# Kernel tuning notes

Hardware: AMD Instinct MI355X
Metric: run time of the kernel (lower is better)

## Reference

```python
import jax, jax.numpy as jnp
import numpy as np

PC_RANGE = [-51.2, -51.2, -5.0, 51.2, 51.2, 3.0]
NUM_HEADS, NUM_LEVELS, NUM_REFS, NUM_POINTS = 8, 4, 4, 1
EPS = 1e-5


def setup_inputs():
    key = jax.random.key(0)
    ks = jax.random.split(key, 16)
    B, CAMS, NQ, C, R = 1, 6, 10000, 256, NUM_REFS
    H, L, P = NUM_HEADS, NUM_LEVELS, NUM_POINTS
    shapes = np.array([[64, 160], [32, 80], [16, 40], [8, 20]], dtype=np.int64)
    hw = shapes[:, 0] * shapes[:, 1]
    lsi = np.concatenate([[0], np.cumsum(hw)[:-1]]).astype(np.int64)
    NK = int(hw.sum())

    def p(k, shape):
        return 0.02 * jax.random.normal(k, shape, jnp.float32)

    return {
        'query': jax.random.normal(ks[0], (NQ, B, C), jnp.float32),
        'query_pos': jax.random.normal(ks[1], (NQ, B, C), jnp.float32),
        'value': jax.random.normal(ks[2], (NK, B * CAMS, C), jnp.float32),
        'bev_reference_points': jax.random.uniform(ks[3], (B, NQ, R, 3), jnp.float32),
        'lidar2img': jax.random.normal(ks[4], (B, CAMS, 3, 4), jnp.float32),
        'img_shape': jnp.broadcast_to(jnp.array([512.0, 960.0], jnp.float32), (B, CAMS, 2)),
        'spatial_shapes': jnp.asarray(shapes),
        'level_start_index': jnp.asarray(lsi),
        'W_val': p(ks[5], (C, C)), 'b_val': jnp.zeros((C,), jnp.float32),
        'W_samp': p(ks[6], (C, H * L * R * P * 2)), 'b_samp': p(ks[7], (H * L * R * P * 2,)),
        'W_attn': p(ks[8], (C, H * L * R * P)), 'b_attn': jnp.zeros((H * L * R * P,), jnp.float32),
        'W_dout': p(ks[9], (C, C)), 'b_dout': jnp.zeros((C,), jnp.float32),
        'W_out': p(ks[10], (C, C)), 'b_out': jnp.zeros((C,), jnp.float32),
    }


def reference(query, query_pos, value, bev_reference_points, lidar2img, img_shape,
              spatial_shapes, level_start_index,
              W_val, b_val, W_samp, b_samp, W_attn, b_attn, W_dout, b_dout, W_out, b_out):
    shapes = np.asarray(spatial_shapes)
    lsi = np.asarray(level_start_index)
    H, L, R, P = NUM_HEADS, NUM_LEVELS, NUM_REFS, NUM_POINTS
    identity = query                                   # (NQ,B,C)
    q = jnp.transpose(query + query_pos, (1, 0, 2))    # (B,NQ,C)
    v = jnp.transpose(value, (1, 0, 2))                # (Bc,NK,C)
    B, NQ, C = q.shape
    CAMS = lidar2img.shape[1]
    Bc, dh = B * CAMS, C // H
    pc = jnp.asarray(PC_RANGE, q.dtype)

    # ---- project 3D reference points to each camera ----
    l2i = jnp.zeros((B, CAMS, 4, 4), q.dtype).at[..., 3, 3].set(1.0).at[..., :3, :4].set(lidar2img)
    xyz = bev_reference_points * (pc[3:6] - pc[0:3]) + pc[0:3]          # (B,NQ,R,3)
    pts = jnp.concatenate([xyz, jnp.ones_like(xyz[..., :1])], -1).reshape(B, NQ * R, 4)
    cam = jnp.einsum('bcij,bnj->bcni', l2i, pts)                         # (B,CAMS,NQ*R,4)
    z = cam[..., 2]
    xy = cam[..., :2] / jnp.maximum(z, EPS)[..., None]
    xy = xy / img_shape[:, :, None, ::-1]                                # x/w, y/h
    mask = (z > EPS) & (xy[..., 0] > 0.) & (xy[..., 0] < 1.) & (xy[..., 1] > 0.) & (xy[..., 1] < 1.)
    mask = mask.reshape(B, CAMS, NQ, R)
    ref_cam = xy.reshape(B, CAMS, NQ, R, 2)

    # rebatch: run attention for all queries per camera, mask outputs (same math as
    # gather-only-valid since deformable attention is pointwise per query)
    q_rb = jnp.broadcast_to(q[:, None], (B, CAMS, NQ, C)).reshape(Bc, NQ, C)
    rp_rb = ref_cam.reshape(Bc, NQ, R, 2)

    # ---- multi-scale deformable attention ----
    vproj = jnp.transpose((v @ W_val + b_val).reshape(Bc, -1, H, dh), (0, 2, 1, 3))  # (Bc,H,NK,dh)
    off = (q_rb @ W_samp + b_samp).reshape(Bc, NQ, H, L, R, P, 2)
    aw = jax.nn.softmax((q_rb @ W_attn + b_attn).reshape(Bc, NQ, H, L * R * P), -1)
    aw = aw.reshape(Bc, NQ, H, L, R, P)
    norm = jnp.asarray(shapes[:, ::-1].copy(), q.dtype)                  # (L,2) = (w,h)
    loc = rp_rb[:, :, None, None, :, None, :] + off / norm[None, None, None, :, None, None, :]

    acc = jnp.zeros((Bc, H, NQ, dh), q.dtype)
    for l in range(L):
        Hl, Wl, s = int(shapes[l, 0]), int(shapes[l, 1]), int(lsi[l])
        vf = vproj[:, :, s:s + Hl * Wl]                                  # (Bc,H,Hl*Wl,dh)

        def rs(t):  # (Bc,NQ,H,R,P) -> (Bc,H,M)
            return jnp.transpose(t, (0, 2, 1, 3, 4)).reshape(Bc, H, NQ * R * P)
        x = rs(loc[:, :, :, l, :, :, 0]) * Wl - 0.5   # grid_sample align_corners=False
        y = rs(loc[:, :, :, l, :, :, 1]) * Hl - 0.5
        w = rs(aw[:, :, :, l])
        x0 = jnp.floor(x); y0 = jnp.floor(y)
        lx = x - x0; ly = y - y0
        ix = x0.astype(jnp.int32); iy = y0.astype(jnp.int32)

        def g(iy_, ix_):  # zero-padding gather
            inb = (iy_ >= 0) & (iy_ < Hl) & (ix_ >= 0) & (ix_ < Wl)
            idx = jnp.clip(iy_, 0, Hl - 1) * Wl + jnp.clip(ix_, 0, Wl - 1)
            return jnp.take_along_axis(vf, idx[..., None], axis=2) * inb[..., None].astype(q.dtype)
        samp = (g(iy, ix) * ((1 - ly) * (1 - lx) * w)[..., None]
                + g(iy, ix + 1) * ((1 - ly) * lx * w)[..., None]
                + g(iy + 1, ix) * (ly * (1 - lx) * w)[..., None]
                + g(iy + 1, ix + 1) * (ly * lx * w)[..., None])            # (Bc,H,M,dh)
        acc = acc + samp.reshape(Bc, H, NQ, R * P, dh).sum(3)
    attn_out = jnp.transpose(acc, (0, 2, 1, 3)).reshape(Bc, NQ, C) @ W_dout + b_dout

    # ---- scatter/average valid camera contributions back to BEV slots ----
    valid = jnp.any(mask, -1)                                            # (B,CAMS,NQ)
    slots = jnp.sum(attn_out.reshape(B, CAMS, NQ, C) * valid[..., None].astype(q.dtype), 1)
    count = jnp.maximum(valid.sum(1).astype(q.dtype), 1.0)               # (B,NQ)
    slots = (slots / count[..., None]) @ W_out + b_out
    return jnp.transpose(slots, (1, 0, 2)) + identity
```

## Files before the change

### kernel.cpp

```cpp
#include <hip/hip_runtime.h>
#include <hip/hip_bf16.h>

namespace {

typedef unsigned short u16;
typedef unsigned int u32;
typedef unsigned char u8;
typedef __attribute__((ext_vector_type(8))) short bf16x8;
typedef __attribute__((ext_vector_type(4))) float f32x4;
typedef __attribute__((ext_vector_type(2))) float f32x2;

constexpr int kNQ   = 10000;
constexpr int kCams = 6;
constexpr int kC    = 256;
constexpr int kNK   = 13600;
constexpr float kEps = 1e-5f;

__device__ __forceinline__ u16 f2b(float f) {
  union { __hip_bfloat16 h; u16 u; } cv;
  cv.h = __float2bfloat16(f);
  return cv.u;
}
__device__ __forceinline__ float b2f(u16 b) {
  return __uint_as_float(((u32)b) << 16);
}
__device__ __forceinline__ bf16x8 pack8(const float4& a, const float4& b) {
  bf16x8 v;
  v[0] = (short)f2b(a.x); v[1] = (short)f2b(a.y);
  v[2] = (short)f2b(a.z); v[3] = (short)f2b(a.w);
  v[4] = (short)f2b(b.x); v[5] = (short)f2b(b.y);
  v[6] = (short)f2b(b.z); v[7] = (short)f2b(b.w);
  return v;
}
__device__ __forceinline__ u8 f2fp8(float v) {
  const u32 t = __builtin_amdgcn_cvt_pk_fp8_f32(v, 0.f, 0u, false);
  return (u8)(t & 0xffu);
}

__global__ __launch_bounds__(256) void k_cvt_w_all(
    const float* __restrict__ w_val, const float* __restrict__ w_samp,
    const float* __restrict__ w_attn, const float* __restrict__ w_dout,
    const float* __restrict__ w_out, u16* __restrict__ t_val,
    u16* __restrict__ t_sa, u16* __restrict__ t_dout, u16* __restrict__ t_out) {
  __shared__ float t[32][33];
  const int bn = blockIdx.x;
  const int bk = blockIdx.y;
  const int tid = threadIdx.x;
  const float* W; u16* Wt; int N, lb;
  if (bn < 8)       { W = w_val;  Wt = t_val;            N = 256; lb = bn; }
  else if (bn < 16) { W = w_samp; Wt = t_sa;             N = 256; lb = bn - 8; }
  else if (bn < 20) { W = w_attn; Wt = t_sa + 256 * 256; N = 128; lb = bn - 16; }
  else if (bn < 28) { W = w_dout; Wt = t_dout;           N = 256; lb = bn - 20; }
  else              { W = w_out;  Wt = t_out;            N = 256; lb = bn - 28; }
#pragma unroll
  for (int e = 0; e < 4; ++e) {
    const int i = e * 256 + tid;
    const int kk = i >> 5, nn = i & 31;
    t[kk][nn] = W[(bk * 32 + kk) * N + lb * 32 + nn];
  }
  __syncthreads();
#pragma unroll
  for (int e = 0; e < 4; ++e) {
    const int i = e * 256 + tid;
    const int nn = i >> 5, kk = i & 31;
    Wt[(lb * 32 + nn) * 256 + bk * 32 + kk] = f2b(t[kk][nn]);
  }
}

__global__ __launch_bounds__(256) void k_cvt_add(const float* __restrict__ a,
                                                 const float* __restrict__ b,
                                                 u16* __restrict__ out) {
  const int t = blockIdx.x * 256 + threadIdx.x;
  const int i = t * 8;
  const float4 x0 = *reinterpret_cast<const float4*>(a + i);
  const float4 x1 = *reinterpret_cast<const float4*>(a + i + 4);
  const float4 y0 = *reinterpret_cast<const float4*>(b + i);
  const float4 y1 = *reinterpret_cast<const float4*>(b + i + 4);
  float4 s0, s1;
  s0.x = x0.x + y0.x; s0.y = x0.y + y0.y; s0.z = x0.z + y0.z; s0.w = x0.w + y0.w;
  s1.x = x1.x + y1.x; s1.y = x1.y + y1.y; s1.z = x1.z + y1.z; s1.w = x1.w + y1.w;
  *reinterpret_cast<bf16x8*>(out + i) = pack8(s0, s1);
}

template <bool OUT_BF16, bool HAS_ADD>
__global__ __launch_bounds__(256) void k_mfma(const u16* __restrict__ A,
                                              const u16* __restrict__ Wt,
                                              const float* __restrict__ bias,
                                              const float* __restrict__ bias2,
                                              int nsplit,
                                              const float* __restrict__ bias_scale,
                                              const float* __restrict__ addend,
                                              void* __restrict__ outp,
                                              int M, int Ntot) {
  __shared__ u16 As[128 * 64];
  __shared__ u16 Bs[128 * 64];
  const int tid = threadIdx.x;
  const int m0 = blockIdx.x * 128;
  const int n0 = blockIdx.y * 128;
  const int wave = tid >> 6;
  const int lane = tid & 63;
  const int wr = wave >> 1;
  const int wc = wave & 1;
  const int lr = lane & 15;
  const int lg = lane >> 4;
  const int srow = tid >> 3;
  const int slot = tid & 7;

  const u16* aptr[4];
  const u16* bptr[4];
  int soff[4];
#pragma unroll
  for (int c = 0; c < 4; ++c) {
    const int rowA = c * 32 + srow;
    const int ra = min(m0 + rowA, M - 1);
    aptr[c] = A + (long long)ra * 256 + slot * 8;
    bptr[c] = Wt + (long long)(n0 + rowA) * 256 + slot * 8;
    soff[c] = rowA * 64 + ((slot ^ (rowA & 7)) << 3);
  }

  f32x4 acc[4][4] = {};

  bf16x8 ca[4], cb[4];
#pragma unroll
  for (int c = 0; c < 4; ++c) {
    ca[c] = *reinterpret_cast<const bf16x8*>(aptr[c]);
    cb[c] = *reinterpret_cast<const bf16x8*>(bptr[c]);
  }

#pragma unroll
  for (int kt = 0; kt < 4; ++kt) {
    bf16x8 na[4], nb[4];
    if (kt < 3) {
      const int k1 = (kt + 1) * 64;
#pragma unroll
      for (int c = 0; c < 4; ++c) {
        na[c] = *reinterpret_cast<const bf16x8*>(aptr[c] + k1);
        nb[c] = *reinterpret_cast<const bf16x8*>(bptr[c] + k1);
      }
    }
#pragma unroll
    for (int c = 0; c < 4; ++c) {
      *reinterpret_cast<bf16x8*>(&As[soff[c]]) = ca[c];
      *reinterpret_cast<bf16x8*>(&Bs[soff[c]]) = cb[c];
    }
    __syncthreads();
#pragma unroll
    for (int ks = 0; ks < 2; ++ks) {
      bf16x8 af[4], bfr[4];
#pragma unroll
      for (int mi = 0; mi < 4; ++mi) {
        const int r = wr * 64 + mi * 16 + lr;
        const int s = ks * 4 + lg;
        af[mi] = *reinterpret_cast<const bf16x8*>(&As[r * 64 + ((s ^ (r & 7)) << 3)]);
      }
#pragma unroll
      for (int ni = 0; ni < 4; ++ni) {
        const int r = wc * 64 + ni * 16 + lr;
        const int s = ks * 4 + lg;
        bfr[ni] = *reinterpret_cast<const bf16x8*>(&Bs[r * 64 + ((s ^ (r & 7)) << 3)]);
      }
#pragma unroll
      for (int mi = 0; mi < 4; ++mi)
#pragma unroll
        for (int ni = 0; ni < 4; ++ni)
          acc[mi][ni] = __builtin_amdgcn_mfma_f32_16x16x32_bf16(af[mi], bfr[ni],
                                                                acc[mi][ni], 0, 0, 0);
    }
    if (kt < 3) {
      __syncthreads();
#pragma unroll
      for (int c = 0; c < 4; ++c) { ca[c] = na[c]; cb[c] = nb[c]; }
    }
  }

#pragma unroll
  for (int mi = 0; mi < 4; ++mi) {
#pragma unroll
    for (int reg = 0; reg < 4; ++reg) {
      const int row = m0 + wr * 64 + mi * 16 + lg * 4 + reg;
      if (row < M) {
        const float bs = bias_scale ? bias_scale[row] : 1.f;
#pragma unroll
        for (int ni = 0; ni < 4; ++ni) {
          const int col = n0 + wc * 64 + ni * 16 + lr;
          const float b = (bias2 && col >= nsplit) ? bias2[col - nsplit] : bias[col];
          float v = acc[mi][ni][reg] + b * bs;
          if (HAS_ADD) v += addend[(long long)row * Ntot + col];
          if (OUT_BF16)
            ((u16*)outp)[(long long)row * Ntot + col] = f2b(v);
          else
            ((float*)outp)[(long long)row * Ntot + col] = v;
        }
      }
    }
  }
}

__global__ __launch_bounds__(256) void k_mfma_vproj(const float* __restrict__ value,
                                                    const u16* __restrict__ Wt,
                                                    const float* __restrict__ bias,
                                                    u8* __restrict__ outp) {
  constexpr int M = kNK * kCams;
  __shared__ u16 As[128 * 64];
  __shared__ u16 Bs[128 * 64];
  const int tid = threadIdx.x;
  const int m0 = blockIdx.x * 128;
  const int n0 = blockIdx.y * 128;
  const int wave = tid >> 6;
  const int lane = tid & 63;
  const int wr = wave >> 1;
  const int wc = wave & 1;
  const int lr = lane & 15;
  const int lg = lane >> 4;
  const int srow = tid >> 3;
  const int slot = tid & 7;

  const float* aptr[4];
  const u16* bptr[4];
  int soff[4];
#pragma unroll
  for (int c = 0; c < 4; ++c) {
    const int rowA = c * 32 + srow;
    const int g = min(m0 + rowA, M - 1);
    const int cam = g / kNK;
    const int n = g - cam * kNK;
    aptr[c] = value + (long long)(n * kCams + cam) * 256 + slot * 8;
    bptr[c] = Wt + (long long)(n0 + rowA) * 256 + slot * 8;
    soff[c] = rowA * 64 + ((slot ^ (rowA & 7)) << 3);
  }

  f32x4 acc[4][4] = {};

  float4 caf[8];
  bf16x8 cb[4];
#pragma unroll
  for (int c = 0; c < 4; ++c) {
    caf[2 * c]     = *reinterpret_cast<const float4*>(aptr[c]);
    caf[2 * c + 1] = *reinterpret_cast<const float4*>(aptr[c] + 4);
    cb[c] = *reinterpret_cast<const bf16x8*>(bptr[c]);
  }

#pragma unroll
  for (int kt = 0; kt < 4; ++kt) {
    float4 naf[8];
    bf16x8 nb[4];
    if (kt < 3) {
      const int k1 = (kt + 1) * 64;
#pragma unroll
      for (int c = 0; c < 4; ++c) {
        naf[2 * c]     = *reinterpret_cast<const float4*>(aptr[c] + k1);
        naf[2 * c + 1] = *reinterpret_cast<const float4*>(aptr[c] + k1 + 4);
        nb[c] = *reinterpret_cast<const bf16x8*>(bptr[c] + k1);
      }
    }
#pragma unroll
    for (int c = 0; c < 4; ++c) {
      *reinterpret_cast<bf16x8*>(&As[soff[c]]) = pack8(caf[2 * c], caf[2 * c + 1]);
      *reinterpret_cast<bf16x8*>(&Bs[soff[c]]) = cb[c];
    }
    __syncthreads();
#pragma unroll
    for (int ks = 0; ks < 2; ++ks) {
      bf16x8 af[4], bfr[4];
#pragma unroll
      for (int mi = 0; mi < 4; ++mi) {
        const int r = wr * 64 + mi * 16 + lr;
        const int s = ks * 4 + lg;
        af[mi] = *reinterpret_cast<const bf16x8*>(&As[r * 64 + ((s ^ (r & 7)) << 3)]);
      }
#pragma unroll
      for (int ni = 0; ni < 4; ++ni) {
        const int r = wc * 64 + ni * 16 + lr;
        const int s = ks * 4 + lg;
        bfr[ni] = *reinterpret_cast<const bf16x8*>(&Bs[r * 64 + ((s ^ (r & 7)) << 3)]);
      }
#pragma unroll
      for (int mi = 0; mi < 4; ++mi)
#pragma unroll
        for (int ni = 0; ni < 4; ++ni)
          acc[mi][ni] = __builtin_amdgcn_mfma_f32_16x16x32_bf16(af[mi], bfr[ni],
                                                                acc[mi][ni], 0, 0, 0);
    }
    if (kt < 3) {
      __syncthreads();
#pragma unroll
      for (int c = 0; c < 4; ++c) {
        caf[2 * c] = naf[2 * c];
        caf[2 * c + 1] = naf[2 * c + 1];
        cb[c] = nb[c];
      }
    }
  }

#pragma unroll
  for (int mi = 0; mi < 4; ++mi) {
#pragma unroll
    for (int reg = 0; reg < 4; ++reg) {
      const int row = m0 + wr * 64 + mi * 16 + lg * 4 + reg;
      if (row < M) {
#pragma unroll
        for (int ni = 0; ni < 4; ++ni) {
          const int col = n0 + wc * 64 + ni * 16 + lr;
          outp[(long long)row * 256 + col] = f2fp8(acc[mi][ni][reg] + bias[col]);
        }
      }
    }
  }
}

__global__ __launch_bounds__(128) void k_softmax16(float* __restrict__ offaw) {
  const int nq = blockIdx.x;
  const int t = threadIdx.x;
  float* p = offaw + (long long)nq * 384 + 256 + t;
  float v = *p;
  float mx = v;
#pragma unroll
  for (int s = 1; s < 16; s <<= 1) mx = fmaxf(mx, __shfl_xor(mx, s));
  const float e = expf(v - mx);
  float sm = e;
#pragma unroll
  for (int s = 1; s < 16; s <<= 1) sm += __shfl_xor(sm, s);
  *p = e / sm;
}

__global__ __launch_bounds__(256) void k_proj_ref(const float* __restrict__ refpts,
                                                  const float* __restrict__ l2i,
                                                  const float* __restrict__ img_shape,
                                                  float* __restrict__ refcam,
                                                  float* __restrict__ valid) {
  const int idx = blockIdx.x * blockDim.x + threadIdx.x;
  if (idx >= kCams * kNQ) return;
  const int cam = idx / kNQ;
  const int nq = idx - cam * kNQ;
  const float* Mp = l2i + cam * 12;
  float m[12];
#pragma unroll
  for (int i = 0; i < 12; ++i) m[i] = Mp[i];
  const float ih = img_shape[cam * 2 + 0];
  const float iw = img_shape[cam * 2 + 1];
  float anyv = 0.f;
  float* rcout = refcam + (long long)idx * 8;
#pragma unroll
  for (int r = 0; r < 4; ++r) {
    const float* rp = refpts + ((long long)nq * 4 + r) * 3;
    const float X = rp[0] * 102.4f + (-51.2f);
    const float Y = rp[1] * 102.4f + (-51.2f);
    const float Z = rp[2] * 8.0f + (-5.0f);
    const float cx = m[0] * X + m[1] * Y + m[2] * Z + m[3];
    const float cy = m[4] * X + m[5] * Y + m[6] * Z + m[7];
    const float cz = m[8] * X + m[9] * Y + m[10] * Z + m[11];
    const float zc = fmaxf(cz, kEps);
    const float xn = cx / zc / iw;
    const float yn = cy / zc / ih;
    rcout[r * 2 + 0] = xn;
    rcout[r * 2 + 1] = yn;
    if ((cz > kEps) && (xn > 0.f) && (xn < 1.f) && (yn > 0.f) && (yn < 1.f)) anyv = 1.f;
  }
  valid[idx] = anyv;
}

__global__ __launch_bounds__(64) void k_sample(const u8* __restrict__ vproj,
                                               const float* __restrict__ refcam,
                                               const float* __restrict__ offaw,
                                               const float* __restrict__ valid,
                                               u16* __restrict__ pre,
                                               float* __restrict__ cflag) {
  const int nq = blockIdx.x;
  const int lane = threadIdx.x;
  const int h = lane >> 3;
  const int d4 = lane & 7;

  static constexpr int SHH[4] = {64, 32, 16, 8};
  static constexpr int SHW[4] = {160, 80, 40, 20};
  static constexpr int LSI[4] = {0, 10240, 12800, 13440};

  const float* offp = offaw + (long long)nq * 384 + h * 32;
  const float* awp = offaw + (long long)nq * 384 + 256 + h * 16;

  float vl[kCams];
#pragma unroll
  for (int c = 0; c < kCams; ++c) vl[c] = valid[c * kNQ + nq];

  float4 acc4 = {0.f, 0.f, 0.f, 0.f};
  float count = 0.f;

  for (int cam = 0; cam < kCams; ++cam) {
    if (vl[cam] == 0.f) continue;
    count += 1.f;

    const float* rcp = refcam + (long long)(cam * kNQ + nq) * 8;
    const float4 rcA = *reinterpret_cast<const float4*>(rcp);
    const float4 rcB = *reinterpret_cast<const float4*>(rcp + 4);
    const float rx[4] = {rcA.x, rcA.z, rcB.x, rcB.z};
    const float ry[4] = {rcA.y, rcA.w, rcB.y, rcB.w};

#pragma unroll
    for (int l = 0; l < 4; ++l) {
      const int Hl = SHH[l];
      const int Wl = SHW[l];
      const float Hf = (float)Hl;
      const float Wf = (float)Wl;
      const float4 aw4 = *reinterpret_cast<const float4*>(awp + l * 4);
      const float4 ofA = *reinterpret_cast<const float4*>(offp + l * 8);
      const float4 ofB = *reinterpret_cast<const float4*>(offp + l * 8 + 4);
      const u8* vf = vproj + ((long long)(cam * kNK + LSI[l])) * 256 + h * 32 + d4 * 4;

      const float ox[4] = {ofA.x, ofA.z, ofB.x, ofB.z};
      const float oy[4] = {ofA.y, ofA.w, ofB.y, ofB.w};
      const float wr[4] = {aw4.x, aw4.y, aw4.z, aw4.w};

#pragma unroll
      for (int r = 0; r < 4; ++r) {
        const float x = fmaf(rx[r], Wf, ox[r]) - 0.5f;
        const float y = fmaf(ry[r], Hf, oy[r]) - 0.5f;
        const float x0 = floorf(x);
        const float y0 = floorf(y);
        const float lx = x - x0;
        const float ly = y - y0;
        const int ix = (int)x0;
        const int iy = (int)y0;
        const int ix0 = min(max(ix, 0), Wl - 1);
        const int ix1 = min(max(ix + 1, 0), Wl - 1);
        const int iy0 = min(max(iy, 0), Hl - 1);
        const int iy1 = min(max(iy + 1, 0), Hl - 1);
        const bool bx0 = (ix >= 0) & (ix < Wl);
        const bool bx1 = (ix >= -1) & (ix + 1 < Wl);
        const bool by0 = (iy >= 0) & (iy < Hl);
        const bool by1 = (iy >= -1) & (iy + 1 < Hl);
        const float w = wr[r];
        const float wy0 = w * (1.f - ly);
        const float wy1 = w * ly;
        const float w00 = (by0 && bx0) ? wy0 * (1.f - lx) : 0.f;
        const float w01 = (by0 && bx1) ? wy0 * lx : 0.f;
        const float w10 = (by1 && bx0) ? wy1 * (1.f - lx) : 0.f;
        const float w11 = (by1 && bx1) ? wy1 * lx : 0.f;
        const int q00 = *reinterpret_cast<const u32*>(vf + (iy0 * Wl + ix0) * 256);
        const int q01 = *reinterpret_cast<const u32*>(vf + (iy0 * Wl + ix1) * 256);
        const int q10 = *reinterpret_cast<const u32*>(vf + (iy1 * Wl + ix0) * 256);
        const int q11 = *reinterpret_cast<const u32*>(vf + (iy1 * Wl + ix1) * 256);
        const f32x2 a00 = __builtin_amdgcn_cvt_pk_f32_fp8(q00, false);
        const f32x2 b00 = __builtin_amdgcn_cvt_pk_f32_fp8(q00, true);
        const f32x2 a01 = __builtin_amdgcn_cvt_pk_f32_fp8(q01, false);
        const f32x2 b01 = __builtin_amdgcn_cvt_pk_f32_fp8(q01, true);
        const f32x2 a10 = __builtin_amdgcn_cvt_pk_f32_fp8(q10, false);
        const f32x2 b10 = __builtin_amdgcn_cvt_pk_f32_fp8(q10, true);
        const f32x2 a11 = __builtin_amdgcn_cvt_pk_f32_fp8(q11, false);
        const f32x2 b11 = __builtin_amdgcn_cvt_pk_f32_fp8(q11, true);
        acc4.x = fmaf(w00, a00[0], fmaf(w01, a01[0], fmaf(w10, a10[0], fmaf(w11, a11[0], acc4.x))));
        acc4.y = fmaf(w00, a00[1], fmaf(w01, a01[1], fmaf(w10, a10[1], fmaf(w11, a11[1], acc4.y))));
        acc4.z = fmaf(w00, b00[0], fmaf(w01, b01[0], fmaf(w10, b10[0], fmaf(w11, b11[0], acc4.z))));
        acc4.w = fmaf(w00, b00[1], fmaf(w01, b01[1], fmaf(w10, b10[1], fmaf(w11, b11[1], acc4.w))));
      }
    }
  }

  const float inv = count > 0.f ? (1.f / count) : 0.f;
  ushort4 o;
  o.x = f2b(acc4.x * inv);
  o.y = f2b(acc4.y * inv);
  o.z = f2b(acc4.z * inv);
  o.w = f2b(acc4.w * inv);
  *reinterpret_cast<ushort4*>(pre + (long long)nq * kC + h * 32 + d4 * 4) = o;
  if (lane == 0) cflag[nq] = count > 0.f ? 1.f : 0.f;
}

}

extern "C" void kernel_launch(void* const* d_in, const int* in_sizes, int n_in,
                              void* d_out, int out_size, void* d_ws, size_t ws_size,
                              hipStream_t stream) {
  (void)in_sizes; (void)n_in; (void)out_size; (void)ws_size;
  const float* query     = (const float*)d_in[0];
  const float* query_pos = (const float*)d_in[1];
  const float* value     = (const float*)d_in[2];
  const float* refpts    = (const float*)d_in[3];
  const float* l2i       = (const float*)d_in[4];
  const float* img_shape = (const float*)d_in[5];
  const float* W_val  = (const float*)d_in[8];
  const float* b_val  = (const float*)d_in[9];
  const float* W_samp = (const float*)d_in[10];
  const float* b_samp = (const float*)d_in[11];
  const float* W_attn = (const float*)d_in[12];
  const float* b_attn = (const float*)d_in[13];
  const float* W_dout = (const float*)d_in[14];
  const float* b_dout = (const float*)d_in[15];
  const float* W_out  = (const float*)d_in[16];
  const float* b_out  = (const float*)d_in[17];

  char* p = (char*)d_ws;
  float* offaw  = (float*)p;  p += 15360000;
  float* refcam = (float*)p;  p += 1920000;
  float* valid  = (float*)p;  p += 240000;
  float* cflag  = (float*)p;  p += 40000;
  u8*    vproj  = (u8*)p;     p += 20889600;
  u16*   pre    = (u16*)p;    p += 5120000;
  u16*   slots  = (u16*)p;    p += 5120000;
  u16*   qpq    = (u16*)p;    p += 5120000;
  u16*   WtVal  = (u16*)p;    p += 131072;
  u16*   WtSA   = (u16*)p;    p += 196608;
  u16*   WtDout = (u16*)p;    p += 131072;
  u16*   WtOut  = (u16*)p;    p += 131072;
  float* out    = (float*)d_out;

  k_cvt_w_all<<<dim3(36, 8), 256, 0, stream>>>(W_val, W_samp, W_attn, W_dout, W_out,
                                               WtVal, WtSA, WtDout, WtOut);

  k_cvt_add<<<dim3(1250), 256, 0, stream>>>(query, query_pos, qpq);

  k_proj_ref<<<dim3((kCams * kNQ + 255) / 256), 256, 0, stream>>>(refpts, l2i,
                                                                  img_shape, refcam,
                                                                  valid);

  k_mfma<false, false><<<dim3(79, 3), 256, 0, stream>>>(
      qpq, WtSA, b_samp, b_attn, 256, nullptr, nullptr, offaw, kNQ, 384);
  k_softmax16<<<dim3(kNQ), 128, 0, stream>>>(offaw);

  k_mfma_vproj<<<dim3(638, 2), 256, 0, stream>>>(value, WtVal, b_val, vproj);

  k_sample<<<dim3(kNQ), 64, 0, stream>>>(vproj, refcam, offaw, valid, pre, cflag);

  k_mfma<true, false><<<dim3(79, 2), 256, 0, stream>>>(
      pre, WtDout, b_dout, nullptr, 0, cflag, nullptr, slots, kNQ, 256);

  k_mfma<false, true><<<dim3(79, 2), 256, 0, stream>>>(
      slots, WtOut, b_out, nullptr, 0, nullptr, query, out, kNQ, 256);
}
```

Before: 132.0 us.

## Double-buffer value projection via direct global-to-LDS loads with full-N tiles

The value projection GEMM now uses global_load_lds to copy fp32 activations and bf16 weights straight into double-buffered, XOR-swizzled shared memory, converting A to bf16 only when fragments are read. Each block now covers all 256 output columns, which halves the grid and avoids reading the fp32 value rows twice. This is meant to overlap memory traffic with MFMA work and cut redundant A loads. In exchange it uses far more LDS (about 128KB, so one block per CU) and more accumulator registers per thread, and it repeats the fp32-to-bf16 conversion for every fragment read.

```diff
diff --git a/kernel.cpp b/kernel.cpp
--- a/kernel.cpp
+++ b/kernel.cpp
@@ -32,9 +32,22 @@
   v[6] = (short)f2b(b.z); v[7] = (short)f2b(b.w);
   return v;
 }
+__device__ __forceinline__ bf16x8 cvt8(const f32x4 lo, const f32x4 hi) {
+  bf16x8 v;
+  v[0] = (short)f2b(lo[0]); v[1] = (short)f2b(lo[1]);
+  v[2] = (short)f2b(lo[2]); v[3] = (short)f2b(lo[3]);
+  v[4] = (short)f2b(hi[0]); v[5] = (short)f2b(hi[1]);
+  v[6] = (short)f2b(hi[2]); v[7] = (short)f2b(hi[3]);
+  return v;
+}
 __device__ __forceinline__ u8 f2fp8(float v) {
   const u32 t = __builtin_amdgcn_cvt_pk_fp8_f32(v, 0.f, 0u, false);
   return (u8)(t & 0xffu);
+}
+__device__ __forceinline__ void gload16(const void* g, void* l) {
+  __builtin_amdgcn_global_load_lds(
+      (const __attribute__((address_space(1))) void*)g,
+      (__attribute__((address_space(3))) void*)l, 16, 0, 0);
 }
 
 __global__ __launch_bounds__(256) void k_cvt_w_all(
@@ -196,100 +209,89 @@
   }
 }
 
-__global__ __launch_bounds__(256) void k_mfma_vproj(const float* __restrict__ value,
-                                                    const u16* __restrict__ Wt,
-                                                    const float* __restrict__ bias,
-                                                    u8* __restrict__ outp) {
+__global__ __launch_bounds__(256, 1) void k_mfma_vproj(
+    const float* __restrict__ value, const u16* __restrict__ Wt,
+    const float* __restrict__ bias, u8* __restrict__ outp) {
   constexpr int M = kNK * kCams;
-  __shared__ u16 As[128 * 64];
-  __shared__ u16 Bs[128 * 64];
+  __shared__ float AsF[2][128 * 64];
+  __shared__ u16  BsH[2][256 * 64];
   const int tid = threadIdx.x;
   const int m0 = blockIdx.x * 128;
-  const int n0 = blockIdx.y * 128;
   const int wave = tid >> 6;
   const int lane = tid & 63;
   const int wr = wave >> 1;
   const int wc = wave & 1;
   const int lr = lane & 15;
   const int lg = lane >> 4;
-  const int srow = tid >> 3;
-  const int slot = tid & 7;
-
-  const float* aptr[4];
-  const u16* bptr[4];
-  int soff[4];
-#pragma unroll
-  for (int c = 0; c < 4; ++c) {
-    const int rowA = c * 32 + srow;
-    const int g = min(m0 + rowA, M - 1);
+
+  const float* asrc[8];
+#pragma unroll
+  for (int i = 0; i < 8; ++i) {
+    const int r = i * 16 + (tid >> 4);
+    const int g = min(m0 + r, M - 1);
     const int cam = g / kNK;
     const int n = g - cam * kNK;
-    aptr[c] = value + (long long)(n * kCams + cam) * 256 + slot * 8;
-    bptr[c] = Wt + (long long)(n0 + rowA) * 256 + slot * 8;
-    soff[c] = rowA * 64 + ((slot ^ (rowA & 7)) << 3);
-  }
-
-  f32x4 acc[4][4] = {};
-
-  float4 caf[8];
-  bf16x8 cb[4];
-#pragma unroll
-  for (int c = 0; c < 4; ++c) {
-    caf[2 * c]     = *reinterpret_cast<const float4*>(aptr[c]);
-    caf[2 * c + 1] = *reinterpret_cast<const float4*>(aptr[c] + 4);
-    cb[c] = *reinterpret_cast<const bf16x8*>(bptr[c]);
-  }
+    const int c = (tid & 15) ^ ((r & 7) << 1);
+    asrc[i] = value + (long long)(n * kCams + cam) * 256 + c * 4;
+  }
+  const u16* bsrc[8];
+#pragma unroll
+  for (int j = 0; j < 8; ++j) {
+    const int rb = j * 32 + (tid >> 3);
+    const int c2 = (tid & 7) ^ (rb & 7);
+    bsrc[j] = Wt + (long long)rb * 256 + c2 * 8;
+  }
+
+  f32x4 acc[4][8] = {};
+
+#pragma unroll
+  for (int i = 0; i < 8; ++i)
+    gload16(asrc[i], (char*)(&AsF[0][0]) + i * 4096 + wave * 1024);
+#pragma unroll
+  for (int j = 0; j < 8; ++j)
+    gload16(bsrc[j], (char*)(&BsH[0][0]) + j * 4096 + wave * 1024);
+  __syncthreads();
 
 #pragma unroll
   for (int kt = 0; kt < 4; ++kt) {
-    float4 naf[8];
-    bf16x8 nb[4];
+    const int buf = kt & 1;
     if (kt < 3) {
-      const int k1 = (kt + 1) * 64;
-#pragma unroll
-      for (int c = 0; c < 4; ++c) {
-        naf[2 * c]     = *reinterpret_cast<const float4*>(aptr[c] + k1);
-        naf[2 * c + 1] = *reinterpret_cast<const float4*>(aptr[c] + k1 + 4);
-        nb[c] = *reinterpret_cast<const bf16x8*>(bptr[c] + k1);
-      }
-    }
-#pragma unroll
-    for (int c = 0; c < 4; ++c) {
-      *reinterpret_cast<bf16x8*>(&As[soff[c]]) = pack8(caf[2 * c], caf[2 * c + 1]);
-      *reinterpret_cast<bf16x8*>(&Bs[soff[c]]) = cb[c];
-    }
-    __syncthreads();
+      const int ko = (kt + 1) * 64;
+#pragma unroll
+      for (int i = 0; i < 8; ++i)
+        gload16(asrc[i] + ko, (char*)(&AsF[buf ^ 1][0]) + i * 4096 + wave * 1024);
+#pragma unroll
+      for (int j = 0; j < 8; ++j)
+        gload16(bsrc[j] + ko, (char*)(&BsH[buf ^ 1][0]) + j * 4096 + wave * 1024);
+    }
+    const float* Ab = &AsF[buf][0];
+    const u16* Bb = &BsH[buf][0];
 #pragma unroll
     for (int ks = 0; ks < 2; ++ks) {
-      bf16x8 af[4], bfr[4];
+      bf16x8 af[4];
 #pragma unroll
       for (int mi = 0; mi < 4; ++mi) {
         const int r = wr * 64 + mi * 16 + lr;
-        const int s = ks * 4 + lg;
-        af[mi] = *reinterpret_cast<const bf16x8*>(&As[r * 64 + ((s ^ (r & 7)) << 3)]);
-      }
-#pragma unroll
-      for (int ni = 0; ni < 4; ++ni) {
-        const int r = wc * 64 + ni * 16 + lr;
-        const int s = ks * 4 + lg;
-        bfr[ni] = *reinterpret_cast<const bf16x8*>(&Bs[r * 64 + ((s ^ (r & 7)) << 3)]);
+        const int off = (ks * 8 + lg * 2) ^ ((r & 7) << 1);
+        const f32x4 lo = *reinterpret_cast<const f32x4*>(Ab + r * 64 + off * 4);
+        const f32x4 hi = *reinterpret_cast<const f32x4*>(Ab + r * 64 + off * 4 + 4);
+        af[mi] = cvt8(lo, hi);
+      }
+      bf16x8 bfr[8];
+#pragma unroll
+      for (int ni = 0; ni < 8; ++ni) {
+        const int rb = wc * 128 + ni * 16 + lr;
+        const int off = (ks * 4 + lg) ^ (rb & 7);
+        bfr[ni] = *reinterpret_cast<const bf16x8*>(Bb + rb * 64 + off * 8);
       }
 #pragma unroll
       for (int mi = 0; mi < 4; ++mi)
 #pragma unroll
-        for (int ni = 0; ni < 4; ++ni)
+        for (int ni = 0; ni < 8; ++ni)
           acc[mi][ni] = __builtin_amdgcn_mfma_f32_16x16x32_bf16(af[mi], bfr[ni],
                                                                 acc[mi][ni], 0, 0, 0);
     }
-    if (kt < 3) {
-      __syncthreads();
-#pragma unroll
-      for (int c = 0; c < 4; ++c) {
-        caf[2 * c] = naf[2 * c];
-        caf[2 * c + 1] = naf[2 * c + 1];
-        cb[c] = nb[c];
-      }
-    }
+    if (kt < 3) __syncthreads();
   }
 
 #pragma unroll
@@ -299,8 +301,8 @@
       const int row = m0 + wr * 64 + mi * 16 + lg * 4 + reg;
       if (row < M) {
 #pragma unroll
-        for (int ni = 0; ni < 4; ++ni) {
-          const int col = n0 + wc * 64 + ni * 16 + lr;
+        for (int ni = 0; ni < 8; ++ni) {
+          const int col = wc * 128 + ni * 16 + lr;
           outp[(long long)row * 256 + col] = f2fp8(acc[mi][ni][reg] + bias[col]);
         }
       }
@@ -515,7 +517,7 @@
       qpq, WtSA, b_samp, b_attn, 256, nullptr, nullptr, offaw, kNQ, 384);
   k_softmax16<<<dim3(kNQ), 128, 0, stream>>>(offaw);
 
-  k_mfma_vproj<<<dim3(638, 2), 256, 0, stream>>>(value, WtVal, b_val, vproj);
+  k_mfma_vproj<<<dim3(638), 256, 0, stream>>>(value, WtVal, b_val, vproj);
 
   k_sample<<<dim3(kNQ), 64, 0, stream>>>(vproj, refcam, offaw, valid, pre, cflag);
 
```

Result: slower. 142.2 us (+7.7%).
